# Kernel tuning notes

Hardware: AMD Instinct MI355X
Metric: run time of the kernel (lower is better)

Reference implementation:

```python
import jax, jax.numpy as jnp
import numpy as np

B, N, L, D, DI = 128, 64, 33, 512, 768  # batch, num_images, cooccurrence_num+1, CLIP dim, inst dim


def setup_inputs() -> dict:
    key = jax.random.key(0)
    ks = jax.random.split(key, 8)
    return {
        "image_features": jax.random.normal(ks[0], (B, N, D), jnp.float32),
        "image_mask": jax.random.randint(ks[1], (B, N), 0, 2).astype(jnp.int32),
        "landmark_feature": jax.random.normal(ks[2], (B, L, D), jnp.float32),
        "inst": jax.random.normal(ks[3], (B, DI), jnp.float32),
        # scoring_module = Linear(512+768 -> 512) -> ReLU -> LayerNorm(512) -> Dropout(eval: identity)
        "W_score": jax.random.normal(ks[4], (DI + D, D), jnp.float32) * 0.02,
        "b_score": jnp.zeros((D,), jnp.float32),
        "ln_gamma": jnp.ones((D,), jnp.float32),
        "ln_beta": jnp.zeros((D,), jnp.float32),
    }


def _l2norm(x):
    return x / jnp.linalg.norm(x, axis=-1, keepdims=True)


def reference(image_features, image_mask, landmark_feature, inst,
              W_score, b_score, ln_gamma, ln_beta):
    LN_EPS = 1e-12
    mask = image_mask == 1  # [B, N]

    img = _l2norm(image_features)          # [B, N, D]
    lmk = _l2norm(landmark_feature)        # [B, L, D]
    img = jnp.where(mask[:, :, None], img, 0.0)
    img_mean = img.mean(axis=1)            # [B, D]

    # scoring_module on cat([inst, img_mean]) -> ReLU -> LayerNorm (Dropout is identity in eval)
    h = jnp.concatenate([inst, img_mean], axis=-1) @ W_score + b_score  # [B, D]
    h = jax.nn.relu(h)
    mu = h.mean(axis=-1, keepdims=True)
    var = h.var(axis=-1, keepdims=True)    # biased, as in torch LayerNorm
    h = (h - mu) / jnp.sqrt(var + LN_EPS) * ln_gamma + ln_beta
    inst_feat = _l2norm(h)                 # [B, D]

    cooccurrence_weight = 100.0 * jnp.einsum('bd,bld->bl', inst_feat, lmk)  # [B, L]
    candidate_prob = 100.0 * jnp.einsum('bnd,bld->bnl', img, lmk)           # [B, N, L]
    candidate_prob = jnp.where(mask[:, :, None], candidate_prob, -jnp.inf)
    p = jax.nn.softmax(candidate_prob, axis=1)                              # softmax over images

    corrected_landmark_feature = jnp.einsum('bnl,bl,bld->bnd', p, cooccurrence_weight, lmk)  # [B, N, D]
    corrected_candidate_prob = jnp.einsum('bnl,bl->bn', p, cooccurrence_weight)              # [B, N]
    corrected_candidate_prob = jnp.where(mask, corrected_candidate_prob, -jnp.inf)
    return corrected_landmark_feature, corrected_candidate_prob
```

## Files before the change

kernel.cpp:

```cpp
#include <hip/hip_runtime.h>
#include <math.h>

#define BB 128
#define NN 64
#define LL 33
#define DD 512
#define DIN 768

#define NEG_BIG (-3.0e38f)

typedef __attribute__((ext_vector_type(8))) short bf16x8;
typedef __attribute__((ext_vector_type(4))) float f32x4;

#define WS_ASW   0
#define WS_BSW   (WS_ASW + BB*3*16*64*4)
#define WS_LMK16 (WS_BSW + BB*4*16*64*4)
#define WS_MEANP (WS_LMK16 + BB*LL*DD/2)
#define WS_PART  (WS_MEANP + BB*4*DD)
#define WS_S     (WS_PART + BB*16*DD)

__device__ __forceinline__ float wave_sum(float v) {
#pragma unroll
  for (int m = 32; m; m >>= 1) v += __shfl_xor(v, m);
  return v;
}
__device__ __forceinline__ float wave_max(float v) {
#pragma unroll
  for (int m = 32; m; m >>= 1) v = fmaxf(v, __shfl_xor(v, m));
  return v;
}
__device__ __forceinline__ unsigned f2bf(float f) {
  unsigned u = __float_as_uint(f);
  return (u + 0x7FFFu + ((u >> 16) & 1u)) >> 16;
}
__device__ __forceinline__ unsigned pk2(float a, float b) {
  return f2bf(a) | (f2bf(b) << 16);
}
__device__ __forceinline__ float bflo(unsigned u) { return __uint_as_float(u << 16); }
__device__ __forceinline__ float bfhi(unsigned u) { return __uint_as_float(u & 0xFFFF0000u); }

__global__ __launch_bounds__(256) void k_prep_v16(
    const float* __restrict__ img_in, const int* __restrict__ mask,
    const float* __restrict__ lmk_in, const float* __restrict__ inst,
    const float* __restrict__ W, unsigned int* __restrict__ AswW,
    unsigned int* __restrict__ BswW, unsigned short* __restrict__ lmk16,
    float* __restrict__ meanp, float* __restrict__ part) {
  __shared__ __align__(16) float shbuf[2048];
  int t = threadIdx.x;

  if (blockIdx.x < 512) {
    uint4* Asw = (uint4*)AswW;
    uint4* Bsw = (uint4*)BswW;
    int o = blockIdx.x;
    int blk = (o & 7) * 64 + (o >> 3);
    int b = blk >> 2, q = blk & 3;
    int w = t >> 6, lane = t & 63;

    int nbase = q * 16 + w * 4;
    const float4* ib = (const float4*)(img_in + ((size_t)b * NN + nbase) * DD);
    float4 r[4][2];
#pragma unroll
    for (int i = 0; i < 4; i++) {
      r[i][0] = ib[i * 128 + lane * 2];
      r[i][1] = ib[i * 128 + lane * 2 + 1];
    }
    const int* mb = mask + b * NN + nbase;
    float macc[8];
#pragma unroll
    for (int j = 0; j < 8; j++) macc[j] = 0.f;
#pragma unroll
    for (int i = 0; i < 4; i++) {
      float4 v0 = r[i][0], v1 = r[i][1];
      float ss = v0.x * v0.x + v0.y * v0.y + v0.z * v0.z + v0.w * v0.w +
                 v1.x * v1.x + v1.y * v1.y + v1.z * v1.z + v1.w * v1.w;
      ss = wave_sum(ss);
      float keep = (mb[i] == 1) ? 1.f : 0.f;
      float s = keep / sqrtf(ss);
      v0.x *= s; v0.y *= s; v0.z *= s; v0.w *= s;
      v1.x *= s; v1.y *= s; v1.z *= s; v1.w *= s;
      macc[0] += v0.x; macc[1] += v0.y; macc[2] += v0.z; macc[3] += v0.w;
      macc[4] += v1.x; macc[5] += v1.y; macc[6] += v1.z; macc[7] += v1.w;
      int rg = nbase + i;
      uint4 p = make_uint4(pk2(v0.x, v0.y), pk2(v0.z, v0.w), pk2(v1.x, v1.y),
                           pk2(v1.z, v1.w));
      Bsw[(((size_t)b * 4 + (rg >> 4)) * 16 + (lane >> 2)) * 64 + (rg & 15) +
          16 * (lane & 3)] = p;
    }
    {
      float4 m0 = {macc[0], macc[1], macc[2], macc[3]};
      float4 m1 = {macc[4], macc[5], macc[6], macc[7]};
      *(float4*)&shbuf[w * 512 + lane * 8] = m0;
      *(float4*)&shbuf[w * 512 + lane * 8 + 4] = m1;
    }
    __syncthreads();
    {
      float s0 = shbuf[t] + shbuf[512 + t] + shbuf[1024 + t] + shbuf[1536 + t];
      float s1 = shbuf[t + 256] + shbuf[512 + t + 256] + shbuf[1024 + t + 256] +
                 shbuf[1536 + t + 256];
      meanp[((size_t)b * 4 + q) * DD + t] = s0;
      meanp[((size_t)b * 4 + q) * DD + t + 256] = s1;
    }

    int lr = q * 8 + w * 2;
    bool xtra = (q == 0) && (w == 3);
    if (xtra) {
#pragma unroll
      for (int kk = 0; kk < 16; kk++)
        if (lane & 15)
          Asw[(((size_t)b * 3 + 2) * 16 + kk) * 64 + lane] =
              make_uint4(0, 0, 0, 0);
    }
#pragma unroll
    for (int k = 0; k < 3; k++) {
      int row = (k < 2) ? (lr + k) : 32;
      if (k == 2 && !xtra) break;
      const float4* lb = (const float4*)(lmk_in + ((size_t)b * LL + row) * DD);
      float4 v0 = lb[lane * 2], v1 = lb[lane * 2 + 1];
      float ss = v0.x * v0.x + v0.y * v0.y + v0.z * v0.z + v0.w * v0.w +
                 v1.x * v1.x + v1.y * v1.y + v1.z * v1.z + v1.w * v1.w;
      ss = wave_sum(ss);
      float s = 1.f / sqrtf(ss);
      v0.x *= s; v0.y *= s; v0.z *= s; v0.w *= s;
      v1.x *= s; v1.y *= s; v1.z *= s; v1.w *= s;
      uint4 p = make_uint4(pk2(v0.x, v0.y), pk2(v0.z, v0.w), pk2(v1.x, v1.y),
                           pk2(v1.z, v1.w));
      ((uint4*)lmk16)[((size_t)b * LL + row) * 64 + lane] = p;
      Asw[(((size_t)b * 3 + (row >> 4)) * 16 + (lane >> 2)) * 64 + (row & 15) +
          16 * (lane & 3)] = p;
    }
  } else {
    float(*xs)[4] = (float(*)[4])shbuf;
    int g = blockIdx.x - 512;
    int gs = (g & 7) * 32 + (g >> 3);
    int bg = gs >> 3, c = gs & 7;
    int b0 = bg * 4;
    int k0 = c * 96;
    for (int i = t; i < 96 * 4; i += 256) {
      int kk = i >> 2;
      int j = i & 3;
      xs[kk][j] = inst[(size_t)(b0 + j) * DIN + k0 + kk];
    }
    __syncthreads();
    const float2* Wp = (const float2*)(W + (size_t)k0 * DD);
    float2 a0 = {0.f, 0.f}, a1 = {0.f, 0.f}, a2 = {0.f, 0.f}, a3 = {0.f, 0.f};
#pragma unroll 4
    for (int kk = 0; kk < 96; kk++) {
      float2 w = Wp[kk * 256 + t];
      float4 xv = *(const float4*)&xs[kk][0];
      a0.x += xv.x * w.x; a0.y += xv.x * w.y;
      a1.x += xv.y * w.x; a1.y += xv.y * w.y;
      a2.x += xv.z * w.x; a2.y += xv.z * w.y;
      a3.x += xv.w * w.x; a3.y += xv.w * w.y;
    }
    float2* pp = (float2*)part;
    pp[(((size_t)(b0 + 0) * 16 + c) * DD >> 1) + t] = a0;
    pp[(((size_t)(b0 + 1) * 16 + c) * DD >> 1) + t] = a1;
    pp[(((size_t)(b0 + 2) * 16 + c) * DD >> 1) + t] = a2;
    pp[(((size_t)(b0 + 3) * 16 + c) * DD >> 1) + t] = a3;
  }
}

__global__ __launch_bounds__(256) void k_gbot_v16(
    const float* __restrict__ meanp, const float* __restrict__ W,
    float* __restrict__ part) {
  __shared__ float xs[64][4];
  int o = blockIdx.x;
  int gs = (o & 7) * 32 + (o >> 3);
  int bg = gs >> 3, c = gs & 7;
  int b0 = bg * 4;
  int t = threadIdx.x;
  int kloc0 = c * 64;
  if (t < 64 * 4) {
    int kk = t >> 2;
    int j = t & 3;
    const float* mp = meanp + (size_t)(b0 + j) * 4 * DD + kloc0 + kk;
    xs[kk][j] = (mp[0] + mp[DD] + mp[2 * DD] + mp[3 * DD]) * (1.f / 64.f);
  }
  __syncthreads();
  const float2* Wp = (const float2*)(W + (size_t)(DIN + kloc0) * DD);
  float2 a0 = {0.f, 0.f}, a1 = {0.f, 0.f}, a2 = {0.f, 0.f}, a3 = {0.f, 0.f};
#pragma unroll 4
  for (int kk = 0; kk < 64; kk++) {
    float2 w = Wp[kk * 256 + t];
    float4 xv = *(const float4*)&xs[kk][0];
    a0.x += xv.x * w.x; a0.y += xv.x * w.y;
    a1.x += xv.y * w.x; a1.y += xv.y * w.y;
    a2.x += xv.z * w.x; a2.y += xv.z * w.y;
    a3.x += xv.w * w.x; a3.y += xv.w * w.y;
  }
  float2* pp = (float2*)part;
  pp[(((size_t)(b0 + 0) * 16 + 8 + c) * DD >> 1) + t] = a0;
  pp[(((size_t)(b0 + 1) * 16 + 8 + c) * DD >> 1) + t] = a1;
  pp[(((size_t)(b0 + 2) * 16 + 8 + c) * DD >> 1) + t] = a2;
  pp[(((size_t)(b0 + 3) * 16 + 8 + c) * DD >> 1) + t] = a3;
}

__device__ __forceinline__ float blk_sum2(float v, float* red4, int t) {
  v = wave_sum(v);
  __syncthreads();
  if ((t & 63) == 0) red4[t >> 6] = v;
  __syncthreads();
  return red4[0] + red4[1] + red4[2] + red4[3];
}

__global__ __launch_bounds__(256) void k_ssm_v16(
    const unsigned int* __restrict__ AswW, const unsigned int* __restrict__ BswW,
    const float* __restrict__ part, const float* __restrict__ bias,
    const float* __restrict__ gamma, const float* __restrict__ beta,
    const unsigned short* __restrict__ lmk16, const int* __restrict__ mask,
    float* __restrict__ q) {
  __shared__ float st[16][68];
  __shared__ float fi[DD];
  __shared__ float red4[4];
  const bf16x8* Asw = (const bf16x8*)AswW;
  const bf16x8* Bsw = (const bf16x8*)BswW;
  int o = blockIdx.x;
  int blk = (o & 7) * 48 + (o >> 3);
  int b = blk / 3, mt = blk - b * 3;
  int t = threadIdx.x;
  int nt = t >> 6, lane = t & 63;

  {
    const float* pb = part + (size_t)b * 16 * DD;
    float sa = 0.f, sb = 0.f;
#pragma unroll
    for (int c = 0; c < 16; c++) {
      sa += pb[c * DD + t];
      sb += pb[c * DD + t + 256];
    }
    float rva = fmaxf(sa + bias[t], 0.f);
    float rvb = fmaxf(sb + bias[t + 256], 0.f);
    float s1 = blk_sum2(rva + rvb, red4, t);
    float s2 = blk_sum2(rva * rva + rvb * rvb, red4, t);
    float mu = s1 * (1.f / DD);
    float var = s2 * (1.f / DD) - mu * mu;
    float inv = 1.f / sqrtf(var + 1e-12f);
    float ya = (rva - mu) * inv * gamma[t] + beta[t];
    float yb = (rvb - mu) * inv * gamma[t + 256] + beta[t + 256];
    float n2 = blk_sum2(ya * ya + yb * yb, red4, t);
    float rn = 1.f / sqrtf(n2);
    fi[t] = ya * rn;
    fi[t + 256] = yb * rn;
  }

  {
    const bf16x8* ap = Asw + ((size_t)(b * 3 + mt) * 16) * 64 + lane;
    const bf16x8* bp = Bsw + ((size_t)(b * 4 + nt) * 16) * 64 + lane;
    f32x4 acc = {0.f, 0.f, 0.f, 0.f};
#pragma unroll
    for (int kk = 0; kk < 16; kk++)
      acc = __builtin_amdgcn_mfma_f32_16x16x32_bf16(ap[kk * 64], bp[kk * 64],
                                                    acc, 0, 0, 0);
    int col = nt * 16 + (lane & 15);
    int rbase = (lane >> 4) << 2;
#pragma unroll
    for (int reg = 0; reg < 4; reg++) st[rbase + reg][col] = 100.f * acc[reg];
  }
  __syncthreads();

  bool keep = (mask[b * NN + lane] == 1);
  const float4* fi4 = (const float4*)fi;
  float4 f0 = fi4[lane * 2], f1 = fi4[lane * 2 + 1];
#pragma unroll
  for (int j = 0; j < 4; j++) {
    int lrow = nt * 4 + j;
    int l = mt * 16 + lrow;
    if (l >= LL) break;
    float s = st[lrow][lane];
    uint4 u = ((const uint4*)(lmk16 + ((size_t)b * LL + l) * DD))[lane];
    float dp = f0.x * bflo(u.x) + f0.y * bfhi(u.x) + f0.z * bflo(u.y) +
               f0.w * bfhi(u.y) + f1.x * bflo(u.z) + f1.y * bfhi(u.z) +
               f1.z * bflo(u.w) + f1.w * bfhi(u.w);
    dp = wave_sum(dp);
    float cw = 100.f * dp;
    float v = keep ? s : NEG_BIG;
    float mx = wave_max(v);
    float e = keep ? __expf(s - mx) : 0.f;
    float Z = wave_sum(e);
    float sc = (Z > 0.f) ? (cw / Z) : 0.f;
    q[((size_t)b * LL + l) * NN + lane] = e * sc;
  }
}

__global__ void k_out_v16(const float* __restrict__ S,
                          const unsigned short* __restrict__ lmk16,
                          const int* __restrict__ mask,
                          float* __restrict__ out1,
                          float* __restrict__ out2) {
  __shared__ __align__(16) float qs[LL][8];
  int o = blockIdx.x;
  int blk = (o & 7) * 128 + (o >> 3);
  int b = blk >> 3;
  int nt = blk & 7;
  int t = threadIdx.x;
  for (int i = t; i < 8 * LL; i += 256) {
    int l = i >> 3;
    int n_loc = i & 7;
    qs[l][n_loc] = S[((size_t)b * LL + l) * NN + nt * 8 + n_loc];
  }
  __syncthreads();
  if (t < 8) {
    float ssum = 0.f;
#pragma unroll
    for (int l = 0; l < LL; l++) ssum += qs[l][t];
    int n = nt * 8 + t;
    out2[b * NN + n] = (mask[b * NN + n] == 1) ? ssum : NEG_BIG;
  }
  int d0 = t * 2;
  float accx[8], accy[8];
#pragma unroll
  for (int n = 0; n < 8; n++) { accx[n] = 0.f; accy[n] = 0.f; }
  const unsigned short* lmkb = lmk16 + (size_t)b * LL * DD;
#pragma unroll 4
  for (int l = 0; l < LL; l++) {
    unsigned u = *(const unsigned*)(lmkb + (size_t)l * DD + d0);
    float lvx = bflo(u), lvy = bfhi(u);
    float4 q0 = *(const float4*)&qs[l][0];
    float4 q1 = *(const float4*)&qs[l][4];
    accx[0] += q0.x * lvx; accy[0] += q0.x * lvy;
    accx[1] += q0.y * lvx; accy[1] += q0.y * lvy;
    accx[2] += q0.z * lvx; accy[2] += q0.z * lvy;
    accx[3] += q0.w * lvx; accy[3] += q0.w * lvy;
    accx[4] += q1.x * lvx; accy[4] += q1.x * lvy;
    accx[5] += q1.y * lvx; accy[5] += q1.y * lvy;
    accx[6] += q1.z * lvx; accy[6] += q1.z * lvy;
    accx[7] += q1.w * lvx; accy[7] += q1.w * lvy;
  }
#pragma unroll
  for (int n = 0; n < 8; n++) {
    float2 oo = {accx[n], accy[n]};
    *(float2*)&out1[(((size_t)b * NN) + nt * 8 + n) * DD + d0] = oo;
  }
}

extern "C" void kernel_launch(void* const* d_in, const int* in_sizes, int n_in,
                              void* d_out, int out_size, void* d_ws, size_t ws_size,
                              hipStream_t stream) {
  const float* image_features = (const float*)d_in[0];
  const int* image_mask = (const int*)d_in[1];
  const float* landmark = (const float*)d_in[2];
  const float* inst = (const float*)d_in[3];
  const float* W = (const float*)d_in[4];
  const float* bias = (const float*)d_in[5];
  const float* gamma = (const float*)d_in[6];
  const float* beta = (const float*)d_in[7];

  float* ws = (float*)d_ws;
  unsigned int* Asw = (unsigned int*)(ws + WS_ASW);
  unsigned int* Bsw = (unsigned int*)(ws + WS_BSW);
  unsigned short* lmk16 = (unsigned short*)(ws + WS_LMK16);
  float* ws_meanp = ws + WS_MEANP;
  float* ws_part = ws + WS_PART;
  float* ws_S = ws + WS_S;

  float* out1 = (float*)d_out;
  float* out2 = (float*)d_out + (size_t)BB * NN * DD;

  k_prep_v16<<<768, 256, 0, stream>>>(image_features, image_mask, landmark,
                                      inst, W, Asw, Bsw, lmk16, ws_meanp,
                                      ws_part);
  k_gbot_v16<<<256, 256, 0, stream>>>(ws_meanp, W, ws_part);
  k_ssm_v16<<<BB * 3, 256, 0, stream>>>((const unsigned int*)Asw,
                                        (const unsigned int*)Bsw, ws_part, bias,
                                        gamma, beta, lmk16, image_mask, ws_S);
  k_out_v16<<<BB * 8, 256, 0, stream>>>(ws_S, lmk16, image_mask, out1, out2);
}
```

Baseline: 45.53 us.

## Stage swizzled bf16 tiles through LDS, widen inst GEMV batching, vectorize output

The prep kernel now writes its normalized bf16 image and landmark rows into shared memory and then copies them to the swizzled global A/B layouts with contiguous coalesced stores, replacing the scattered 16-byte writes. Landmark normalization is reorganized so blocks with q<2 each handle 16 rows and q==2 handles the last row plus zero padding. The inst-GEMV blocks now process 8 batches per block instead of 4, which halves W reads and cuts that grid from 256 to 128 blocks. The output kernel computes a 4x4 tile per thread with float4 stores instead of 8x2 with float2 stores. The extra syncthreads and larger LDS footprint may lower occupancy.

After: 51.53 us. 13.2% more time.

```diff
diff --git a/kernel.cpp b/kernel.cpp
--- a/kernel.cpp
+++ b/kernel.cpp
@@ -39,18 +39,18 @@
 __device__ __forceinline__ float bflo(unsigned u) { return __uint_as_float(u << 16); }
 __device__ __forceinline__ float bfhi(unsigned u) { return __uint_as_float(u & 0xFFFF0000u); }
 
-__global__ __launch_bounds__(256) void k_prep_v16(
+__global__ __launch_bounds__(256) void k_prep_v17(
     const float* __restrict__ img_in, const int* __restrict__ mask,
     const float* __restrict__ lmk_in, const float* __restrict__ inst,
     const float* __restrict__ W, unsigned int* __restrict__ AswW,
     unsigned int* __restrict__ BswW, unsigned short* __restrict__ lmk16,
     float* __restrict__ meanp, float* __restrict__ part) {
-  __shared__ __align__(16) float shbuf[2048];
+  __shared__ __align__(16) unsigned char smem[16 * 260 * 4 + 4 * 512 * 4];
   int t = threadIdx.x;
 
   if (blockIdx.x < 512) {
-    uint4* Asw = (uint4*)AswW;
-    uint4* Bsw = (uint4*)BswW;
+    unsigned int(*lds16)[260] = (unsigned int(*)[260])smem;
+    float* shm = (float*)(smem + 16 * 260 * 4);
     int o = blockIdx.x;
     int blk = (o & 7) * 64 + (o >> 3);
     int b = blk >> 2, q = blk & 3;
@@ -80,87 +80,125 @@
       v1.x *= s; v1.y *= s; v1.z *= s; v1.w *= s;
       macc[0] += v0.x; macc[1] += v0.y; macc[2] += v0.z; macc[3] += v0.w;
       macc[4] += v1.x; macc[5] += v1.y; macc[6] += v1.z; macc[7] += v1.w;
-      int rg = nbase + i;
       uint4 p = make_uint4(pk2(v0.x, v0.y), pk2(v0.z, v0.w), pk2(v1.x, v1.y),
                            pk2(v1.z, v1.w));
-      Bsw[(((size_t)b * 4 + (rg >> 4)) * 16 + (lane >> 2)) * 64 + (rg & 15) +
-          16 * (lane & 3)] = p;
-    }
-    {
-      float4 m0 = {macc[0], macc[1], macc[2], macc[3]};
-      float4 m1 = {macc[4], macc[5], macc[6], macc[7]};
-      *(float4*)&shbuf[w * 512 + lane * 8] = m0;
-      *(float4*)&shbuf[w * 512 + lane * 8 + 4] = m1;
-    }
+      *(uint4*)&lds16[w * 4 + i][lane * 4] = p;
+    }
+    *(float4*)&shm[w * 512 + lane * 8] =
+        make_float4(macc[0], macc[1], macc[2], macc[3]);
+    *(float4*)&shm[w * 512 + lane * 8 + 4] =
+        make_float4(macc[4], macc[5], macc[6], macc[7]);
     __syncthreads();
     {
-      float s0 = shbuf[t] + shbuf[512 + t] + shbuf[1024 + t] + shbuf[1536 + t];
-      float s1 = shbuf[t + 256] + shbuf[512 + t + 256] + shbuf[1024 + t + 256] +
-                 shbuf[1536 + t + 256];
+      uint4* dstB = (uint4*)BswW + ((size_t)b * 4 + q) * 16 * 64;
+#pragma unroll
+      for (int s4 = 0; s4 < 4; s4++) {
+        int slot = s4 * 256 + t;
+        int kk = slot >> 6, l = slot & 63;
+        dstB[slot] = *(const uint4*)&lds16[l & 15][kk * 16 + (l >> 4) * 4];
+      }
+      float s0 = shm[t] + shm[512 + t] + shm[1024 + t] + shm[1536 + t];
+      float s1 = shm[t + 256] + shm[512 + t + 256] + shm[1024 + t + 256] +
+                 shm[1536 + t + 256];
       meanp[((size_t)b * 4 + q) * DD + t] = s0;
       meanp[((size_t)b * 4 + q) * DD + t + 256] = s1;
     }
-
-    int lr = q * 8 + w * 2;
-    bool xtra = (q == 0) && (w == 3);
-    if (xtra) {
-#pragma unroll
-      for (int kk = 0; kk < 16; kk++)
-        if (lane & 15)
-          Asw[(((size_t)b * 3 + 2) * 16 + kk) * 64 + lane] =
-              make_uint4(0, 0, 0, 0);
-    }
-#pragma unroll
-    for (int k = 0; k < 3; k++) {
-      int row = (k < 2) ? (lr + k) : 32;
-      if (k == 2 && !xtra) break;
-      const float4* lb = (const float4*)(lmk_in + ((size_t)b * LL + row) * DD);
-      float4 v0 = lb[lane * 2], v1 = lb[lane * 2 + 1];
-      float ss = v0.x * v0.x + v0.y * v0.y + v0.z * v0.z + v0.w * v0.w +
-                 v1.x * v1.x + v1.y * v1.y + v1.z * v1.z + v1.w * v1.w;
-      ss = wave_sum(ss);
-      float s = 1.f / sqrtf(ss);
-      v0.x *= s; v0.y *= s; v0.z *= s; v0.w *= s;
-      v1.x *= s; v1.y *= s; v1.z *= s; v1.w *= s;
-      uint4 p = make_uint4(pk2(v0.x, v0.y), pk2(v0.z, v0.w), pk2(v1.x, v1.y),
-                           pk2(v1.z, v1.w));
-      ((uint4*)lmk16)[((size_t)b * LL + row) * 64 + lane] = p;
-      Asw[(((size_t)b * 3 + (row >> 4)) * 16 + (lane >> 2)) * 64 + (row & 15) +
-          16 * (lane & 3)] = p;
+    __syncthreads();
+
+    if (q < 2) {
+      int rbase = q * 16 + w * 4;
+      float4 la[4][2];
+#pragma unroll
+      for (int i = 0; i < 4; i++) {
+        const float4* lb =
+            (const float4*)(lmk_in + ((size_t)b * LL + rbase + i) * DD);
+        la[i][0] = lb[lane * 2];
+        la[i][1] = lb[lane * 2 + 1];
+      }
+#pragma unroll
+      for (int i = 0; i < 4; i++) {
+        float4 v0 = la[i][0], v1 = la[i][1];
+        float ss = v0.x * v0.x + v0.y * v0.y + v0.z * v0.z + v0.w * v0.w +
+                   v1.x * v1.x + v1.y * v1.y + v1.z * v1.z + v1.w * v1.w;
+        ss = wave_sum(ss);
+        float s = 1.f / sqrtf(ss);
+        v0.x *= s; v0.y *= s; v0.z *= s; v0.w *= s;
+        v1.x *= s; v1.y *= s; v1.z *= s; v1.w *= s;
+        uint4 p = make_uint4(pk2(v0.x, v0.y), pk2(v0.z, v0.w), pk2(v1.x, v1.y),
+                             pk2(v1.z, v1.w));
+        ((uint4*)lmk16)[((size_t)b * LL + rbase + i) * 64 + lane] = p;
+        *(uint4*)&lds16[w * 4 + i][lane * 4] = p;
+      }
+    } else if (q == 2) {
+#pragma unroll
+      for (int i = 0; i < 4; i++) {
+        int rr = w * 4 + i;
+        if (rr == 0) {
+          const float4* lb = (const float4*)(lmk_in + ((size_t)b * LL + 32) * DD);
+          float4 v0 = lb[lane * 2], v1 = lb[lane * 2 + 1];
+          float ss = v0.x * v0.x + v0.y * v0.y + v0.z * v0.z + v0.w * v0.w +
+                     v1.x * v1.x + v1.y * v1.y + v1.z * v1.z + v1.w * v1.w;
+          ss = wave_sum(ss);
+          float s = 1.f / sqrtf(ss);
+          v0.x *= s; v0.y *= s; v0.z *= s; v0.w *= s;
+          v1.x *= s; v1.y *= s; v1.z *= s; v1.w *= s;
+          uint4 p = make_uint4(pk2(v0.x, v0.y), pk2(v0.z, v0.w),
+                               pk2(v1.x, v1.y), pk2(v1.z, v1.w));
+          ((uint4*)lmk16)[((size_t)b * LL + 32) * 64 + lane] = p;
+          *(uint4*)&lds16[0][lane * 4] = p;
+        } else {
+          *(uint4*)&lds16[rr][lane * 4] = make_uint4(0, 0, 0, 0);
+        }
+      }
+    }
+    __syncthreads();
+    if (q < 3) {
+      uint4* dstA = (uint4*)AswW + ((size_t)b * 3 + q) * 16 * 64;
+#pragma unroll
+      for (int s4 = 0; s4 < 4; s4++) {
+        int slot = s4 * 256 + t;
+        int kk = slot >> 6, l = slot & 63;
+        dstA[slot] = *(const uint4*)&lds16[l & 15][kk * 16 + (l >> 4) * 4];
+      }
     }
   } else {
-    float(*xs)[4] = (float(*)[4])shbuf;
+    float(*xs)[8] = (float(*)[8])smem;
     int g = blockIdx.x - 512;
-    int gs = (g & 7) * 32 + (g >> 3);
+    int gs = (g & 7) * 16 + (g >> 3);
     int bg = gs >> 3, c = gs & 7;
-    int b0 = bg * 4;
+    int b0 = bg * 8;
     int k0 = c * 96;
-    for (int i = t; i < 96 * 4; i += 256) {
-      int kk = i >> 2;
-      int j = i & 3;
+    for (int i = t; i < 96 * 8; i += 256) {
+      int kk = i >> 3, j = i & 7;
       xs[kk][j] = inst[(size_t)(b0 + j) * DIN + k0 + kk];
     }
     __syncthreads();
     const float2* Wp = (const float2*)(W + (size_t)k0 * DD);
-    float2 a0 = {0.f, 0.f}, a1 = {0.f, 0.f}, a2 = {0.f, 0.f}, a3 = {0.f, 0.f};
-#pragma unroll 4
+    float2 a[8];
+#pragma unroll
+    for (int j = 0; j < 8; j++) a[j] = make_float2(0.f, 0.f);
+#pragma unroll 2
     for (int kk = 0; kk < 96; kk++) {
-      float2 w = Wp[kk * 256 + t];
-      float4 xv = *(const float4*)&xs[kk][0];
-      a0.x += xv.x * w.x; a0.y += xv.x * w.y;
-      a1.x += xv.y * w.x; a1.y += xv.y * w.y;
-      a2.x += xv.z * w.x; a2.y += xv.z * w.y;
-      a3.x += xv.w * w.x; a3.y += xv.w * w.y;
+      float2 wv = Wp[kk * 256 + t];
+      float4 x0 = *(const float4*)&xs[kk][0];
+      float4 x1 = *(const float4*)&xs[kk][4];
+      a[0].x += x0.x * wv.x; a[0].y += x0.x * wv.y;
+      a[1].x += x0.y * wv.x; a[1].y += x0.y * wv.y;
+      a[2].x += x0.z * wv.x; a[2].y += x0.z * wv.y;
+      a[3].x += x0.w * wv.x; a[3].y += x0.w * wv.y;
+      a[4].x += x1.x * wv.x; a[4].y += x1.x * wv.y;
+      a[5].x += x1.y * wv.x; a[5].y += x1.y * wv.y;
+      a[6].x += x1.z * wv.x; a[6].y += x1.z * wv.y;
+      a[7].x += x1.w * wv.x; a[7].y += x1.w * wv.y;
     }
     float2* pp = (float2*)part;
-    pp[(((size_t)(b0 + 0) * 16 + c) * DD >> 1) + t] = a0;
-    pp[(((size_t)(b0 + 1) * 16 + c) * DD >> 1) + t] = a1;
-    pp[(((size_t)(b0 + 2) * 16 + c) * DD >> 1) + t] = a2;
-    pp[(((size_t)(b0 + 3) * 16 + c) * DD >> 1) + t] = a3;
-  }
-}
-
-__global__ __launch_bounds__(256) void k_gbot_v16(
+#pragma unroll
+    for (int j = 0; j < 8; j++)
+      pp[(((size_t)(b0 + j) * 16 + c) * DD >> 1) + t] = a[j];
+  }
+}
+
+__global__ __launch_bounds__(256) void k_gbot_v17(
     const float* __restrict__ meanp, const float* __restrict__ W,
     float* __restrict__ part) {
   __shared__ float xs[64][4];
@@ -203,7 +241,7 @@
   return red4[0] + red4[1] + red4[2] + red4[3];
 }
 
-__global__ __launch_bounds__(256) void k_ssm_v16(
+__global__ __launch_bounds__(256) void k_ssm_v17(
     const unsigned int* __restrict__ AswW, const unsigned int* __restrict__ BswW,
     const float* __restrict__ part, const float* __restrict__ bias,
     const float* __restrict__ gamma, const float* __restrict__ beta,
@@ -282,7 +320,7 @@
   }
 }
 
-__global__ void k_out_v16(const float* __restrict__ S,
+__global__ void k_out_v17(const float* __restrict__ S,
                           const unsigned short* __restrict__ lmk16,
                           const int* __restrict__ mask,
                           float* __restrict__ out1,
@@ -306,30 +344,32 @@
     int n = nt * 8 + t;
     out2[b * NN + n] = (mask[b * NN + n] == 1) ? ssum : NEG_BIG;
   }
-  int d0 = t * 2;
-  float accx[8], accy[8];
-#pragma unroll
-  for (int n = 0; n < 8; n++) { accx[n] = 0.f; accy[n] = 0.f; }
+  int d0 = (t & 127) * 4;
+  int nh = t >> 7;
+  float acc[4][4];
+#pragma unroll
+  for (int n = 0; n < 4; n++)
+#pragma unroll
+    for (int d = 0; d < 4; d++) acc[n][d] = 0.f;
   const unsigned short* lmkb = lmk16 + (size_t)b * LL * DD;
 #pragma unroll 4
   for (int l = 0; l < LL; l++) {
-    unsigned u = *(const unsigned*)(lmkb + (size_t)l * DD + d0);
-    float lvx = bflo(u), lvy = bfhi(u);
-    float4 q0 = *(const float4*)&qs[l][0];
-    float4 q1 = *(const float4*)&qs[l][4];
-    accx[0] += q0.x * lvx; accy[0] += q0.x * lvy;
-    accx[1] += q0.y * lvx; accy[1] += q0.y * lvy;
-    accx[2] += q0.z * lvx; accy[2] += q0.z * lvy;
-    accx[3] += q0.w * lvx; accy[3] += q0.w * lvy;
-    accx[4] += q1.x * lvx; accy[4] += q1.x * lvy;
-    accx[5] += q1.y * lvx; accy[5] += q1.y * lvy;
-    accx[6] += q1.z * lvx; accy[6] += q1.z * lvy;
-    accx[7] += q1.w * lvx; accy[7] += q1.w * lvy;
-  }
-#pragma unroll
-  for (int n = 0; n < 8; n++) {
-    float2 oo = {accx[n], accy[n]};
-    *(float2*)&out1[(((size_t)b * NN) + nt * 8 + n) * DD + d0] = oo;
+    uint2 u = *(const uint2*)(lmkb + (size_t)l * DD + d0);
+    float lv0 = bflo(u.x), lv1 = bfhi(u.x), lv2 = bflo(u.y), lv3 = bfhi(u.y);
+    float4 qv = *(const float4*)&qs[l][nh * 4];
+    acc[0][0] += qv.x * lv0; acc[0][1] += qv.x * lv1;
+    acc[0][2] += qv.x * lv2; acc[0][3] += qv.x * lv3;
+    acc[1][0] += qv.y * lv0; acc[1][1] += qv.y * lv1;
+    acc[1][2] += qv.y * lv2; acc[1][3] += qv.y * lv3;
+    acc[2][0] += qv.z * lv0; acc[2][1] += qv.z * lv1;
+    acc[2][2] += qv.z * lv2; acc[2][3] += qv.z * lv3;
+    acc[3][0] += qv.w * lv0; acc[3][1] += qv.w * lv1;
+    acc[3][2] += qv.w * lv2; acc[3][3] += qv.w * lv3;
+  }
+#pragma unroll
+  for (int n = 0; n < 4; n++) {
+    float4 oo = {acc[n][0], acc[n][1], acc[n][2], acc[n][3]};
+    *(float4*)&out1[(((size_t)b * NN) + nt * 8 + nh * 4 + n) * DD + d0] = oo;
   }
 }
 
@@ -356,12 +396,12 @@
   float* out1 = (float*)d_out;
   float* out2 = (float*)d_out + (size_t)BB * NN * DD;
 
-  k_prep_v16<<<768, 256, 0, stream>>>(image_features, image_mask, landmark,
+  k_prep_v17<<<640, 256, 0, stream>>>(image_features, image_mask, landmark,
                                       inst, W, Asw, Bsw, lmk16, ws_meanp,
                                       ws_part);
-  k_gbot_v16<<<256, 256, 0, stream>>>(ws_meanp, W, ws_part);
-  k_ssm_v16<<<BB * 3, 256, 0, stream>>>((const unsigned int*)Asw,
+  k_gbot_v17<<<256, 256, 0, stream>>>(ws_meanp, W, ws_part);
+  k_ssm_v17<<<BB * 3, 256, 0, stream>>>((const unsigned int*)Asw,
                                         (const unsigned int*)Bsw, ws_part, bias,
                                         gamma, beta, lmk16, image_mask, ws_S);
-  k_out_v16<<<BB * 8, 256, 0, stream>>>(ws_S, lmk16, image_mask, out1, out2);
-}
+  k_out_v17<<<BB * 8, 256, 0, stream>>>(ws_S, lmk16, image_mask, out1, out2);
+}
```
